# Kernel optimization log

Measured on AMD Instinct MI355X. Metric: run time of the kernel, lower is better.

## Reference

```python
import jax, jax.numpy as jnp
import numpy as np

N_NODES = 100000
N_EDGES = 640000
WIDTH = 128
LAYERS = 3
N_GRAPHS = 64


def setup_inputs() -> dict:
    key = jax.random.key(0)
    ks = jax.random.split(key, 6)
    x = jax.random.normal(ks[0], (N_NODES, WIDTH), dtype=jnp.float32)
    edge_index = jax.random.randint(ks[1], (2, N_EDGES), 0, N_NODES, dtype=jnp.int64)
    edge_attr = jax.random.uniform(ks[2], (N_EDGES, 1), dtype=jnp.float32)
    batch = jnp.sort(jax.random.randint(ks[3], (N_NODES,), 0, N_GRAPHS, dtype=jnp.int64))
    Ws = jax.random.normal(ks[4], (LAYERS, WIDTH, WIDTH), dtype=jnp.float32) / np.sqrt(WIDTH)
    bs = jnp.zeros((LAYERS, WIDTH), dtype=jnp.float32)
    return {"x": x, "edge_index": edge_index, "edge_attr": edge_attr,
            "batch": batch, "Ws": Ws, "bs": bs}


def reference(x, edge_index, edge_attr, batch, Ws, bs):
    N = x.shape[0]
    ew = edge_attr.squeeze()  # [E]
    loop = jnp.arange(N)
    # add self-loops with fill_value=2.0 (improved=True)
    row = jnp.concatenate([edge_index[0], loop])
    col = jnp.concatenate([edge_index[1], loop])
    w = jnp.concatenate([ew, jnp.full((N,), 2.0, dtype=ew.dtype)])
    # symmetric gcn normalization: deg computed at target (col)
    deg = jax.ops.segment_sum(w, col, num_segments=N)
    dinv = jnp.where(deg > 0, jax.lax.rsqrt(deg), 0.0)
    norm = dinv[row] * w * dinv[col]  # [E+N]

    for l in range(LAYERS):
        h = x @ Ws[l]  # [N, WIDTH]
        msg = norm[:, None] * h[row]  # gather + scale
        x = jax.ops.segment_sum(msg, col, num_segments=N) + bs[l]

    # global mean pool over graphs
    sums = jax.ops.segment_sum(x, batch, num_segments=N_GRAPHS)
    counts = jax.ops.segment_sum(jnp.ones((N,), dtype=x.dtype), batch, num_segments=N_GRAPHS)
    return sums / jnp.maximum(counts, 1.0)[:, None]
```

## Files before the change

kernel.cpp:

```cpp
#include <hip/hip_runtime.h>
#include <hip/hip_fp16.h>
#include <cstddef>

#define N_NODES  100000
#define N_EDGES  640000
#define WIDTH    128
#define LAYERS   3
#define N_GRAPHS 64
#define ELL_K    40

#define GLOAD_LDS16(gsrc, ldst) \
  __builtin_amdgcn_global_load_lds( \
      (const __attribute__((address_space(1))) unsigned*)(gsrc), \
      (__attribute__((address_space(3))) unsigned*)(ldst), 16, 0, 0)

__device__ __forceinline__ float h2f(unsigned short h) {
  __half x; *reinterpret_cast<unsigned short*>(&x) = h;
  return __half2float(x);
}
__device__ __forceinline__ unsigned short f2h(float f) {
  __half h = __float2half_rn(f);
  return *reinterpret_cast<unsigned short*>(&h);
}


__global__ void k_init(int* __restrict__ cursor, float* __restrict__ deg) {
  int i = blockIdx.x * blockDim.x + threadIdx.x;
  if (i < N_NODES) { cursor[i] = 0; deg[i] = 0.f; }
}

__global__ void k_cd(const int* __restrict__ col, const float* __restrict__ ew,
                     float* __restrict__ deg) {
  int e = blockIdx.x * blockDim.x + threadIdx.x;
  if (e < N_EDGES) atomicAdd(&deg[col[e]], ew[e]);
}

__global__ void k_dinv_e(const float* __restrict__ deg, float* __restrict__ dinv) {
  int v = blockIdx.x * blockDim.x + threadIdx.x;
  if (v < N_NODES) {
    float d = 2.0f + deg[v];
    dinv[v] = (d > 0.0f) ? 1.0f / sqrtf(d) : 0.0f;
  }
}

__global__ void k_fill_ell(const int* __restrict__ row, const int* __restrict__ col,
                           const float* __restrict__ ew, const float* __restrict__ dinv,
                           int* __restrict__ cursor, int2* __restrict__ ell) {
  int e = blockIdx.x * blockDim.x + threadIdx.x;
  if (e < N_EDGES) {
    int r = row[e], c = col[e];
    float nrm = dinv[r] * ew[e] * dinv[c];
    int slot = atomicAdd(&cursor[r], 1);
    if (slot < ELL_K) {
      int2 pk; pk.x = c; pk.y = __float_as_int(nrm);
      ell[(size_t)r * ELL_K + slot] = pk;
    }
  }
}

__device__ __forceinline__ int lbound(const int* __restrict__ batch, int key) {
  int lo = 0, hi = N_NODES;
  while (lo < hi) { int m = (lo + hi) >> 1; if (batch[m] < key) lo = m + 1; else hi = m; }
  return lo;
}

__global__ void k_cntg(const int* __restrict__ batch, int* __restrict__ cntg,
                       float* __restrict__ invc) {
  int g = threadIdx.x;
  if (g < N_GRAPHS) {
    int lb = lbound(batch, g), ub = lbound(batch, g + 1);
    int c = ub - lb;
    cntg[g] = c;
    invc[g] = 1.0f / (float)max(c, 1);
  }
}

__global__ void k_pinit(const int* __restrict__ batch, const float* __restrict__ invc,
                        unsigned short* __restrict__ p) {
  const int total = N_NODES * 16;
  for (int i = blockIdx.x * blockDim.x + threadIdx.x; i < total;
       i += gridDim.x * blockDim.x) {
    int v = i >> 4, q = i & 15;
    int b = batch[v];
    ushort4 u;
    ((unsigned short*)&u)[0] = (q * 4 + 0 == b) ? f2h(invc[b]) : (unsigned short)0;
    ((unsigned short*)&u)[1] = (q * 4 + 1 == b) ? f2h(invc[b]) : (unsigned short)0;
    ((unsigned short*)&u)[2] = (q * 4 + 2 == b) ? f2h(invc[b]) : (unsigned short)0;
    ((unsigned short*)&u)[3] = (q * 4 + 3 == b) ? f2h(invc[b]) : (unsigned short)0;
    ((ushort4*)p)[i] = u;
  }
}

#define CS_BLOCKS 512
__global__ __launch_bounds__(256) void k_colsum(
    const unsigned short* __restrict__ y, float* __restrict__ partc) {
  __shared__ float4 sd[256];
  int t = threadIdx.x;
  int slot = t & 15;
  int vrow = t >> 4;
  const int chunk = (N_NODES + CS_BLOCKS - 1) / CS_BLOCKS;
  int start = blockIdx.x * chunk;
  int end = min(start + chunk, N_NODES);
  float4 acc = {0.f, 0.f, 0.f, 0.f};
  for (int v = start + vrow; v < end; v += 16) {
    ushort4 u = ((const ushort4*)(y + (size_t)v * 64))[slot];
    acc.x += h2f(u.x); acc.y += h2f(u.y);
    acc.z += h2f(u.z); acc.w += h2f(u.w);
  }
  sd[t] = acc;
  __syncthreads();
  for (int off = 8; off > 0; off >>= 1) {
    if (vrow < off) {
      float4 o = sd[(vrow + off) * 16 + slot];
      acc.x += o.x; acc.y += o.y; acc.z += o.z; acc.w += o.w;
      sd[t] = acc;
    }
    __syncthreads();
  }
  if (vrow == 0)
    ((float4*)(partc + (size_t)blockIdx.x * 64))[slot] = acc;
}

__global__ __launch_bounds__(256) void k_cs2(
    const float* __restrict__ csA, const float* __restrict__ csB,
    float* __restrict__ ps, float* __restrict__ pas) {
  __shared__ float sd[256];
  const float* src = (blockIdx.x == 0) ? csA : csB;
  float* dst = (blockIdx.x == 0) ? ps : pas;
  int t = threadIdx.x;
  int g = t & 63, c = t >> 6;
  float a = 0.f;
  for (int r = c * 128; r < (c + 1) * 128; r++) a += src[r * 64 + g];
  sd[t] = a;
  __syncthreads();
  if (t < 128) sd[t] += sd[t + 128];
  __syncthreads();
  if (t < 64) dst[t] = sd[t] + sd[t + 64];
}

#define AGG_NPB 4
__global__ __launch_bounds__(256) void k_yagg(
    const unsigned short* __restrict__ yin, const int* __restrict__ cnt_a,
    const int2* __restrict__ ell, const float* __restrict__ dinv,
    unsigned short* __restrict__ yout) {
  int wave = threadIdx.x >> 6;
  int lane = threadIdx.x & 63;
  int v = blockIdx.x * AGG_NPB + wave;
  if (v >= N_NODES) return;
  int vv = __builtin_amdgcn_readfirstlane(v);
  int grp = lane >> 4;
  int q = lane & 15;

  ushort4 hvu = ((const ushort4*)(yin + (size_t)vv * 64))[q];
  int cnt = cnt_a[vv];

  float4 a0 = {0,0,0,0}, a1 = {0,0,0,0}, a2 = {0,0,0,0}, a3 = {0,0,0,0};
  int2 pk = (lane < cnt) ? ell[(size_t)vv * ELL_K + lane] : make_int2(0, 0);
  int   si = pk.x;
  float swv = __int_as_float(pk.y);

  for (int base = 0; base < cnt; base += 16) {
    int e0 = base + grp;
    float w0 = __shfl(swv, e0); int i0 = __shfl(si, e0);
    ushort4 u0 = ((const ushort4*)(yin + (size_t)i0 * 64))[q];
    a0.x += w0 * h2f(u0.x); a0.y += w0 * h2f(u0.y);
    a0.z += w0 * h2f(u0.z); a0.w += w0 * h2f(u0.w);
    if (base + 4 < cnt) {
      int e1 = base + 4 + grp;
      float w1 = __shfl(swv, e1); int i1 = __shfl(si, e1);
      ushort4 u1 = ((const ushort4*)(yin + (size_t)i1 * 64))[q];
      a1.x += w1 * h2f(u1.x); a1.y += w1 * h2f(u1.y);
      a1.z += w1 * h2f(u1.z); a1.w += w1 * h2f(u1.w);
    }
    if (base + 8 < cnt) {
      int e2 = base + 8 + grp;
      int e3 = base + 12 + grp;
      float w2 = __shfl(swv, e2); int i2 = __shfl(si, e2);
      float w3 = __shfl(swv, e3); int i3 = __shfl(si, e3);
      ushort4 u2 = ((const ushort4*)(yin + (size_t)i2 * 64))[q];
      ushort4 u3 = ((const ushort4*)(yin + (size_t)i3 * 64))[q];
      a2.x += w2 * h2f(u2.x); a2.y += w2 * h2f(u2.y);
      a2.z += w2 * h2f(u2.z); a2.w += w2 * h2f(u2.w);
      a3.x += w3 * h2f(u3.x); a3.y += w3 * h2f(u3.y);
      a3.z += w3 * h2f(u3.z); a3.w += w3 * h2f(u3.w);
    }
  }

  a0.x += a1.x + a2.x + a3.x;
  a0.y += a1.y + a2.y + a3.y;
  a0.z += a1.z + a2.z + a3.z;
  a0.w += a1.w + a2.w + a3.w;
#pragma unroll
  for (int d = 16; d <= 32; d <<= 1) {
    a0.x += __shfl_xor(a0.x, d);
    a0.y += __shfl_xor(a0.y, d);
    a0.z += __shfl_xor(a0.z, d);
    a0.w += __shfl_xor(a0.w, d);
  }

  if (grp == 0) {
    float dv = dinv[vv];
    float sc = 2.0f * dv * dv;
    ushort4 r;
    r.x = f2h(a0.x + sc * h2f(hvu.x));
    r.y = f2h(a0.y + sc * h2f(hvu.y));
    r.z = f2h(a0.z + sc * h2f(hvu.z));
    r.w = f2h(a0.w + sc * h2f(hvu.w));
    ((ushort4*)(yout + (size_t)vv * 64))[q] = r;
  }
}

#define CT_BLOCKS 768
#define CT_NCHUNK ((N_NODES + 63) / 64)

__global__ __launch_bounds__(256) void k_contract(
    const float* __restrict__ x0, const unsigned short* __restrict__ y3,
    float* __restrict__ part) {
  __shared__ __align__(16) float xs[64 * 128];
  __shared__ __align__(16) unsigned short ysh[64 * 64];
  int t = threadIdx.x;
  int w = t >> 6;
  int lane = t & 63;
  int j = lane * 2;

  float2 acc[16];
#pragma unroll
  for (int i = 0; i < 16; i++) acc[i] = make_float2(0.f, 0.f);

  for (int c = blockIdx.x; c < CT_NCHUNK; c += gridDim.x) {
    int cc = min(64, N_NODES - c * 64);
    int bx = cc * 512;
    int by = cc * 128;
    const char* gx = (const char*)(x0 + (size_t)c * 64 * 128);
    const char* gy = (const char*)(y3 + (size_t)c * 64 * 64);
    __syncthreads();
#pragma unroll
    for (int i = 0; i < 8; i++) {
      int off = i * 4096 + t * 16;
      if (off < bx) GLOAD_LDS16(gx + off, (char*)xs + off);
    }
#pragma unroll
    for (int i = 0; i < 2; i++) {
      int off = i * 4096 + t * 16;
      if (off < by) GLOAD_LDS16(gy + off, (char*)ysh + off);
    }
    asm volatile("s_waitcnt vmcnt(0)" ::: "memory");
    __syncthreads();

    for (int v = 0; v < cc; v++) {
      const ushort4* yr = (const ushort4*)(ysh + v * 64 + w * 16);
      ushort4 u0 = yr[0], u1 = yr[1], u2 = yr[2], u3 = yr[3];
      float2 xa = *(const float2*)(xs + v * 128 + j);
      float ys[16] = {h2f(u0.x), h2f(u0.y), h2f(u0.z), h2f(u0.w),
                      h2f(u1.x), h2f(u1.y), h2f(u1.z), h2f(u1.w),
                      h2f(u2.x), h2f(u2.y), h2f(u2.z), h2f(u2.w),
                      h2f(u3.x), h2f(u3.y), h2f(u3.z), h2f(u3.w)};
#pragma unroll
      for (int i = 0; i < 16; i++) {
        acc[i].x += ys[i] * xa.x;
        acc[i].y += ys[i] * xa.y;
      }
    }
  }

  float* dst = part + (size_t)blockIdx.x * (N_GRAPHS * WIDTH);
#pragma unroll
  for (int i = 0; i < 16; i++)
    *(float2*)(dst + (w * 16 + i) * WIDTH + j) = acc[i];
}

#define RC_ROWS 64
#define RC_RG (CT_BLOCKS / RC_ROWS)

__global__ __launch_bounds__(256) void k_reduce1(
    const float* __restrict__ part, float* __restrict__ part2) {
  int bid = blockIdx.x, t = threadIdx.x;
  int rg = bid >> 5, colc = bid & 31;
  int idx = colc * 256 + t;
  const float* src = part + (size_t)rg * RC_ROWS * (N_GRAPHS * WIDTH) + idx;
  float a0 = 0.f, a1 = 0.f, a2 = 0.f, a3 = 0.f;
  for (int r = 0; r < RC_ROWS; r += 4) {
    a0 += src[(size_t)(r + 0) * (N_GRAPHS * WIDTH)];
    a1 += src[(size_t)(r + 1) * (N_GRAPHS * WIDTH)];
    a2 += src[(size_t)(r + 2) * (N_GRAPHS * WIDTH)];
    a3 += src[(size_t)(r + 3) * (N_GRAPHS * WIDTH)];
  }
  part2[rg * (N_GRAPHS * WIDTH) + idx] = (a0 + a1) + (a2 + a3);
}

__global__ __launch_bounds__(WIDTH) void k_mm128(
    const float* __restrict__ A, const float* __restrict__ B, float* __restrict__ O) {
  __shared__ float Ar[WIDTH];
  int r = blockIdx.x, j = threadIdx.x;
  Ar[j] = A[r * WIDTH + j];
  __syncthreads();
  float a = 0.f;
#pragma unroll 8
  for (int k = 0; k < WIDTH; k++) a += Ar[k] * B[k * WIDTH + j];
  O[r * WIDTH + j] = a;
}

__global__ __launch_bounds__(WIDTH) void k_c01(
    const float* __restrict__ b0, const float* __restrict__ T1,
    const float* __restrict__ b1, const float* __restrict__ W2,
    float* __restrict__ c0, float* __restrict__ c1) {
  __shared__ float s0[WIDTH], s1v[WIDTH];
  int j = threadIdx.x;
  s0[j] = b0[j]; s1v[j] = b1[j];
  __syncthreads();
  float a0 = 0.f, a1 = 0.f;
#pragma unroll 8
  for (int k = 0; k < WIDTH; k++) {
    a0 += s0[k] * T1[k * WIDTH + j];
    a1 += s1v[k] * W2[k * WIDTH + j];
  }
  c0[j] = a0; c1[j] = a1;
}

__global__ __launch_bounds__(WIDTH) void k_out(
    const float* __restrict__ part2, const float* __restrict__ Wp,
    const float* __restrict__ c0, const float* __restrict__ c1,
    const float* __restrict__ ps, const float* __restrict__ pas,
    const int* __restrict__ cntg, const float* __restrict__ b2,
    float* __restrict__ out) {
  __shared__ float Cr[WIDTH];
  int g = blockIdx.x, j = threadIdx.x;
  float cv = 0.f;
#pragma unroll
  for (int rg = 0; rg < RC_RG; rg++)
    cv += part2[rg * (N_GRAPHS * WIDTH) + g * WIDTH + j];
  Cr[j] = cv;
  __syncthreads();
  float a = pas[g] * c0[j] + ps[g] * c1[j] + ((cntg[g] > 0) ? b2[j] : 0.f);
#pragma unroll 8
  for (int k = 0; k < WIDTH; k++) a += Cr[k] * Wp[k * WIDTH + j];
  out[g * WIDTH + j] = a;
}


extern "C" void kernel_launch(void* const* d_in, const int* in_sizes, int n_in,
                              void* d_out, int out_size, void* d_ws, size_t ws_size,
                              hipStream_t stream) {
  const float* x   = (const float*)d_in[0];
  const int* row   = (const int*)d_in[1];
  const int* col   = row + N_EDGES;
  const float* ew  = (const float*)d_in[2];
  const int* batch = (const int*)d_in[3];
  const float* Ws  = (const float*)d_in[4];
  const float* bs  = (const float*)d_in[5];
  float* out = (float*)d_out;

  char* w = (char*)d_ws;
  float* dinv    = (float*)(w + 0);
  float* deg     = (float*)(w + 400128);
  int*   cursor  = (int*)(w + 800256);
  int*   cntg    = (int*)(w + 1200384);
  float* invc    = (float*)(w + 1200640);
  float* ps      = (float*)(w + 1200896);
  float* pas     = (float*)(w + 1201152);
  float* T1      = (float*)(w + 1201408);
  float* Wp      = (float*)(w + 1266944);
  float* c0      = (float*)(w + 1332480);
  float* c1      = (float*)(w + 1332992);
  int2*  ell     = (int2*)(w + 1333504);
  float* part    = (float*)(w + 33554432);
  float* part2   = (float*)(w + 58720256);
  unsigned short* yA = (unsigned short*)(w + 59113472);
  unsigned short* yB = (unsigned short*)(w + 71913472);
  float* csA     = (float*)(w + 84713472);
  float* csB     = (float*)(w + 84844544);

  int nb_n = (N_NODES + 255) / 256;
  int nb_e = (N_EDGES + 255) / 256;

  k_init  <<<nb_n, 256, 0, stream>>>(cursor, deg);
  k_cd    <<<nb_e, 256, 0, stream>>>(col, ew, deg);
  k_dinv_e<<<nb_n, 256, 0, stream>>>(deg, dinv);
  k_fill_ell<<<nb_e, 256, 0, stream>>>(row, col, ew, dinv, cursor, ell);

  k_cntg <<<1, 64, 0, stream>>>(batch, cntg, invc);
  k_pinit<<<2048, 256, 0, stream>>>(batch, invc, yA);

  int nb_y = (N_NODES + AGG_NPB - 1) / AGG_NPB;
  k_yagg  <<<nb_y, 256, 0, stream>>>(yA, cursor, ell, dinv, yB);
  k_colsum<<<CS_BLOCKS, 256, 0, stream>>>(yB, csA);
  k_yagg  <<<nb_y, 256, 0, stream>>>(yB, cursor, ell, dinv, yA);
  k_colsum<<<CS_BLOCKS, 256, 0, stream>>>(yA, csB);
  k_yagg  <<<nb_y, 256, 0, stream>>>(yA, cursor, ell, dinv, yB);

  k_cs2  <<<2, 256, 0, stream>>>(csA, csB, ps, pas);
  k_mm128<<<WIDTH, WIDTH, 0, stream>>>(Ws + 1 * WIDTH * WIDTH, Ws + 2 * WIDTH * WIDTH, T1);
  k_mm128<<<WIDTH, WIDTH, 0, stream>>>(Ws + 0 * WIDTH * WIDTH, T1, Wp);
  k_c01  <<<1, WIDTH, 0, stream>>>(bs, T1, bs + WIDTH, Ws + 2 * WIDTH * WIDTH, c0, c1);

  k_contract<<<CT_BLOCKS, 256, 0, stream>>>(x, yB, part);
  k_reduce1 <<<RC_RG * 32, 256, 0, stream>>>(part, part2);
  k_out     <<<N_GRAPHS, WIDTH, 0, stream>>>(part2, Wp, c0, c1, ps, pas, cntg,
                                             bs + 2 * WIDTH, out);
}
```

Measured before the change: 288.0 us.

## Factor degree normalization out of edges, fuse ELL build, simplify contraction

Stores raw edge weights in the ELL table and rescales the pooling vectors by dinv so each aggregation applies a single per-node scale (d2 or dinv) instead of per-edge norms. This lets the degree accumulation and the ELL fill share one edge pass, which removes a separate kernel. Column sums are corrected with sqrt(deg). The contraction kernel drops its LDS staging and reads x and y directly per node, two nodes per iteration, with more blocks. The risk is extra fp16 rounding from the changed scaling, plus a larger partial buffer to reduce.

Result: faster. 278.8 us (-3.2%).

```diff
diff --git a/kernel.cpp b/kernel.cpp
--- a/kernel.cpp
+++ b/kernel.cpp
@@ -9,11 +9,6 @@
 #define N_GRAPHS 64
 #define ELL_K    40
 
-#define GLOAD_LDS16(gsrc, ldst) \
-  __builtin_amdgcn_global_load_lds( \
-      (const __attribute__((address_space(1))) unsigned*)(gsrc), \
-      (__attribute__((address_space(3))) unsigned*)(ldst), 16, 0, 0)
-
 __device__ __forceinline__ float h2f(unsigned short h) {
   __half x; *reinterpret_cast<unsigned short*>(&x) = h;
   return __half2float(x);
@@ -29,32 +24,32 @@
   if (i < N_NODES) { cursor[i] = 0; deg[i] = 0.f; }
 }
 
-__global__ void k_cd(const int* __restrict__ col, const float* __restrict__ ew,
-                     float* __restrict__ deg) {
+__global__ void k_fill_cd(const int* __restrict__ row, const int* __restrict__ col,
+                          const float* __restrict__ ew,
+                          int* __restrict__ cursor, float* __restrict__ deg,
+                          int2* __restrict__ ell) {
   int e = blockIdx.x * blockDim.x + threadIdx.x;
-  if (e < N_EDGES) atomicAdd(&deg[col[e]], ew[e]);
-}
-
-__global__ void k_dinv_e(const float* __restrict__ deg, float* __restrict__ dinv) {
+  if (e < N_EDGES) {
+    int r = row[e], c = col[e];
+    float w = ew[e];
+    atomicAdd(&deg[c], w);
+    int slot = atomicAdd(&cursor[r], 1);
+    if (slot < ELL_K) {
+      int2 pk; pk.x = c; pk.y = __float_as_int(w);
+      ell[(size_t)r * ELL_K + slot] = pk;
+    }
+  }
+}
+
+__global__ void k_dinv_e(const float* __restrict__ deg, float* __restrict__ dinv,
+                         float* __restrict__ d2, float* __restrict__ sq) {
   int v = blockIdx.x * blockDim.x + threadIdx.x;
   if (v < N_NODES) {
     float d = 2.0f + deg[v];
-    dinv[v] = (d > 0.0f) ? 1.0f / sqrtf(d) : 0.0f;
-  }
-}
-
-__global__ void k_fill_ell(const int* __restrict__ row, const int* __restrict__ col,
-                           const float* __restrict__ ew, const float* __restrict__ dinv,
-                           int* __restrict__ cursor, int2* __restrict__ ell) {
-  int e = blockIdx.x * blockDim.x + threadIdx.x;
-  if (e < N_EDGES) {
-    int r = row[e], c = col[e];
-    float nrm = dinv[r] * ew[e] * dinv[c];
-    int slot = atomicAdd(&cursor[r], 1);
-    if (slot < ELL_K) {
-      int2 pk; pk.x = c; pk.y = __float_as_int(nrm);
-      ell[(size_t)r * ELL_K + slot] = pk;
-    }
+    float di = (d > 0.0f) ? 1.0f / sqrtf(d) : 0.0f;
+    dinv[v] = di;
+    d2[v] = di * di;
+    sq[v] = sqrtf(d);
   }
 }
 
@@ -76,24 +71,26 @@
 }
 
 __global__ void k_pinit(const int* __restrict__ batch, const float* __restrict__ invc,
-                        unsigned short* __restrict__ p) {
+                        const float* __restrict__ dinv, unsigned short* __restrict__ p) {
   const int total = N_NODES * 16;
   for (int i = blockIdx.x * blockDim.x + threadIdx.x; i < total;
        i += gridDim.x * blockDim.x) {
     int v = i >> 4, q = i & 15;
     int b = batch[v];
+    unsigned short val = f2h(invc[b] * dinv[v]);
     ushort4 u;
-    ((unsigned short*)&u)[0] = (q * 4 + 0 == b) ? f2h(invc[b]) : (unsigned short)0;
-    ((unsigned short*)&u)[1] = (q * 4 + 1 == b) ? f2h(invc[b]) : (unsigned short)0;
-    ((unsigned short*)&u)[2] = (q * 4 + 2 == b) ? f2h(invc[b]) : (unsigned short)0;
-    ((unsigned short*)&u)[3] = (q * 4 + 3 == b) ? f2h(invc[b]) : (unsigned short)0;
+    ((unsigned short*)&u)[0] = (q * 4 + 0 == b) ? val : (unsigned short)0;
+    ((unsigned short*)&u)[1] = (q * 4 + 1 == b) ? val : (unsigned short)0;
+    ((unsigned short*)&u)[2] = (q * 4 + 2 == b) ? val : (unsigned short)0;
+    ((unsigned short*)&u)[3] = (q * 4 + 3 == b) ? val : (unsigned short)0;
     ((ushort4*)p)[i] = u;
   }
 }
 
 #define CS_BLOCKS 512
 __global__ __launch_bounds__(256) void k_colsum(
-    const unsigned short* __restrict__ y, float* __restrict__ partc) {
+    const unsigned short* __restrict__ y, const float* __restrict__ sq,
+    float* __restrict__ partc) {
   __shared__ float4 sd[256];
   int t = threadIdx.x;
   int slot = t & 15;
@@ -104,8 +101,9 @@
   float4 acc = {0.f, 0.f, 0.f, 0.f};
   for (int v = start + vrow; v < end; v += 16) {
     ushort4 u = ((const ushort4*)(y + (size_t)v * 64))[slot];
-    acc.x += h2f(u.x); acc.y += h2f(u.y);
-    acc.z += h2f(u.z); acc.w += h2f(u.w);
+    float rd = sq[v];
+    acc.x += h2f(u.x) * rd; acc.y += h2f(u.y) * rd;
+    acc.z += h2f(u.z) * rd; acc.w += h2f(u.w) * rd;
   }
   sd[t] = acc;
   __syncthreads();
@@ -141,7 +139,7 @@
 #define AGG_NPB 4
 __global__ __launch_bounds__(256) void k_yagg(
     const unsigned short* __restrict__ yin, const int* __restrict__ cnt_a,
-    const int2* __restrict__ ell, const float* __restrict__ dinv,
+    const int2* __restrict__ ell, const float* __restrict__ scale,
     unsigned short* __restrict__ yout) {
   int wave = threadIdx.x >> 6;
   int lane = threadIdx.x & 63;
@@ -199,74 +197,70 @@
   }
 
   if (grp == 0) {
-    float dv = dinv[vv];
-    float sc = 2.0f * dv * dv;
+    float sc = scale[vv];
     ushort4 r;
-    r.x = f2h(a0.x + sc * h2f(hvu.x));
-    r.y = f2h(a0.y + sc * h2f(hvu.y));
-    r.z = f2h(a0.z + sc * h2f(hvu.z));
-    r.w = f2h(a0.w + sc * h2f(hvu.w));
+    r.x = f2h(sc * (a0.x + 2.0f * h2f(hvu.x)));
+    r.y = f2h(sc * (a0.y + 2.0f * h2f(hvu.y)));
+    r.z = f2h(sc * (a0.z + 2.0f * h2f(hvu.z)));
+    r.w = f2h(sc * (a0.w + 2.0f * h2f(hvu.w)));
     ((ushort4*)(yout + (size_t)vv * 64))[q] = r;
   }
 }
 
-#define CT_BLOCKS 768
-#define CT_NCHUNK ((N_NODES + 63) / 64)
+#define CT_BLOCKS 1024
 
 __global__ __launch_bounds__(256) void k_contract(
     const float* __restrict__ x0, const unsigned short* __restrict__ y3,
     float* __restrict__ part) {
-  __shared__ __align__(16) float xs[64 * 128];
-  __shared__ __align__(16) unsigned short ysh[64 * 64];
   int t = threadIdx.x;
-  int w = t >> 6;
-  int lane = t & 63;
-  int j = lane * 2;
-
-  float2 acc[16];
-#pragma unroll
-  for (int i = 0; i < 16; i++) acc[i] = make_float2(0.f, 0.f);
-
-  for (int c = blockIdx.x; c < CT_NCHUNK; c += gridDim.x) {
-    int cc = min(64, N_NODES - c * 64);
-    int bx = cc * 512;
-    int by = cc * 128;
-    const char* gx = (const char*)(x0 + (size_t)c * 64 * 128);
-    const char* gy = (const char*)(y3 + (size_t)c * 64 * 64);
-    __syncthreads();
+  int jq = t & 31;
+  int gg = t >> 5;
+
+  float4 acc[8];
+#pragma unroll
+  for (int i = 0; i < 8; i++) acc[i] = make_float4(0.f, 0.f, 0.f, 0.f);
+
+  int v = blockIdx.x;
+  for (; v + CT_BLOCKS < N_NODES; v += 2 * CT_BLOCKS) {
+    int v2 = v + CT_BLOCKS;
+    float4 xa = ((const float4*)(x0 + (size_t)v * WIDTH))[jq];
+    float4 xb = ((const float4*)(x0 + (size_t)v2 * WIDTH))[jq];
+    const ushort4* ya = (const ushort4*)(y3 + (size_t)v * 64 + gg * 8);
+    const ushort4* yb = (const ushort4*)(y3 + (size_t)v2 * 64 + gg * 8);
+    ushort4 ua0 = ya[0], ua1 = ya[1];
+    ushort4 ub0 = yb[0], ub1 = yb[1];
+    float yas[8] = {h2f(ua0.x), h2f(ua0.y), h2f(ua0.z), h2f(ua0.w),
+                    h2f(ua1.x), h2f(ua1.y), h2f(ua1.z), h2f(ua1.w)};
+    float ybs[8] = {h2f(ub0.x), h2f(ub0.y), h2f(ub0.z), h2f(ub0.w),
+                    h2f(ub1.x), h2f(ub1.y), h2f(ub1.z), h2f(ub1.w)};
 #pragma unroll
     for (int i = 0; i < 8; i++) {
-      int off = i * 4096 + t * 16;
-      if (off < bx) GLOAD_LDS16(gx + off, (char*)xs + off);
-    }
-#pragma unroll
-    for (int i = 0; i < 2; i++) {
-      int off = i * 4096 + t * 16;
-      if (off < by) GLOAD_LDS16(gy + off, (char*)ysh + off);
-    }
-    asm volatile("s_waitcnt vmcnt(0)" ::: "memory");
-    __syncthreads();
-
-    for (int v = 0; v < cc; v++) {
-      const ushort4* yr = (const ushort4*)(ysh + v * 64 + w * 16);
-      ushort4 u0 = yr[0], u1 = yr[1], u2 = yr[2], u3 = yr[3];
-      float2 xa = *(const float2*)(xs + v * 128 + j);
-      float ys[16] = {h2f(u0.x), h2f(u0.y), h2f(u0.z), h2f(u0.w),
-                      h2f(u1.x), h2f(u1.y), h2f(u1.z), h2f(u1.w),
-                      h2f(u2.x), h2f(u2.y), h2f(u2.z), h2f(u2.w),
-                      h2f(u3.x), h2f(u3.y), h2f(u3.z), h2f(u3.w)};
-#pragma unroll
-      for (int i = 0; i < 16; i++) {
-        acc[i].x += ys[i] * xa.x;
-        acc[i].y += ys[i] * xa.y;
-      }
+      acc[i].x += yas[i] * xa.x; acc[i].y += yas[i] * xa.y;
+      acc[i].z += yas[i] * xa.z; acc[i].w += yas[i] * xa.w;
+    }
+#pragma unroll
+    for (int i = 0; i < 8; i++) {
+      acc[i].x += ybs[i] * xb.x; acc[i].y += ybs[i] * xb.y;
+      acc[i].z += ybs[i] * xb.z; acc[i].w += ybs[i] * xb.w;
+    }
+  }
+  if (v < N_NODES) {
+    float4 xa = ((const float4*)(x0 + (size_t)v * WIDTH))[jq];
+    const ushort4* ya = (const ushort4*)(y3 + (size_t)v * 64 + gg * 8);
+    ushort4 ua0 = ya[0], ua1 = ya[1];
+    float yas[8] = {h2f(ua0.x), h2f(ua0.y), h2f(ua0.z), h2f(ua0.w),
+                    h2f(ua1.x), h2f(ua1.y), h2f(ua1.z), h2f(ua1.w)};
+#pragma unroll
+    for (int i = 0; i < 8; i++) {
+      acc[i].x += yas[i] * xa.x; acc[i].y += yas[i] * xa.y;
+      acc[i].z += yas[i] * xa.z; acc[i].w += yas[i] * xa.w;
     }
   }
 
   float* dst = part + (size_t)blockIdx.x * (N_GRAPHS * WIDTH);
 #pragma unroll
-  for (int i = 0; i < 16; i++)
-    *(float2*)(dst + (w * 16 + i) * WIDTH + j) = acc[i];
+  for (int i = 0; i < 8; i++)
+    *(float4*)(dst + (gg * 8 + i) * WIDTH + jq * 4) = acc[i];
 }
 
 #define RC_ROWS 64
@@ -352,40 +346,41 @@
 
   char* w = (char*)d_ws;
   float* dinv    = (float*)(w + 0);
-  float* deg     = (float*)(w + 400128);
-  int*   cursor  = (int*)(w + 800256);
-  int*   cntg    = (int*)(w + 1200384);
-  float* invc    = (float*)(w + 1200640);
-  float* ps      = (float*)(w + 1200896);
-  float* pas     = (float*)(w + 1201152);
-  float* T1      = (float*)(w + 1201408);
-  float* Wp      = (float*)(w + 1266944);
-  float* c0      = (float*)(w + 1332480);
-  float* c1      = (float*)(w + 1332992);
-  int2*  ell     = (int2*)(w + 1333504);
-  float* part    = (float*)(w + 33554432);
-  float* part2   = (float*)(w + 58720256);
-  unsigned short* yA = (unsigned short*)(w + 59113472);
-  unsigned short* yB = (unsigned short*)(w + 71913472);
-  float* csA     = (float*)(w + 84713472);
-  float* csB     = (float*)(w + 84844544);
+  float* d2      = (float*)(w + 400128);
+  float* sq      = (float*)(w + 800256);
+  float* deg     = (float*)(w + 1200384);
+  int*   cursor  = (int*)(w + 1600512);
+  int*   cntg    = (int*)(w + 2000640);
+  float* invc    = (float*)(w + 2000896);
+  float* ps      = (float*)(w + 2001152);
+  float* pas     = (float*)(w + 2001408);
+  float* T1      = (float*)(w + 2001664);
+  float* Wp      = (float*)(w + 2067200);
+  float* c0      = (float*)(w + 2132736);
+  float* c1      = (float*)(w + 2133248);
+  int2*  ell     = (int2*)(w + 2133760);
+  float* part    = (float*)(w + 34133760);
+  float* part2   = (float*)(w + 67688192);
+  unsigned short* yA = (unsigned short*)(w + 68212480);
+  unsigned short* yB = (unsigned short*)(w + 81012480);
+  float* csA     = (float*)(w + 93812480);
+  float* csB     = (float*)(w + 93943552);
 
   int nb_n = (N_NODES + 255) / 256;
   int nb_e = (N_EDGES + 255) / 256;
 
-  k_init  <<<nb_n, 256, 0, stream>>>(cursor, deg);
-  k_cd    <<<nb_e, 256, 0, stream>>>(col, ew, deg);
-  k_dinv_e<<<nb_n, 256, 0, stream>>>(deg, dinv);
-  k_fill_ell<<<nb_e, 256, 0, stream>>>(row, col, ew, dinv, cursor, ell);
+  k_init   <<<nb_n, 256, 0, stream>>>(cursor, deg);
+  k_fill_cd<<<nb_e, 256, 0, stream>>>(row, col, ew, cursor, deg, ell);
+  k_dinv_e <<<nb_n, 256, 0, stream>>>(deg, dinv, d2, sq);
 
   k_cntg <<<1, 64, 0, stream>>>(batch, cntg, invc);
-  k_pinit<<<2048, 256, 0, stream>>>(batch, invc, yA);
+  k_pinit<<<2048, 256, 0, stream>>>(batch, invc, dinv, yA);
 
   int nb_y = (N_NODES + AGG_NPB - 1) / AGG_NPB;
-  k_yagg  <<<nb_y, 256, 0, stream>>>(yA, cursor, ell, dinv, yB);
-  k_colsum<<<CS_BLOCKS, 256, 0, stream>>>(yB, csA);
-  k_yagg  <<<nb_y, 256, 0, stream>>>(yB, cursor, ell, dinv, yA);
-  k_colsum<<<CS_BLOCKS, 256, 0, stream>>>(yA, csB);
+  k_yagg  <<<nb_y, 256, 0, stream>>>(yA, cursor, ell, d2, yB);
+  k_colsum<<<CS_BLOCKS, 256, 0, stream>>>(yB, sq, csA);
+  k_yagg  <<<nb_y, 256, 0, stream>>>(yB, cursor, ell, d2, yA);
+  k_colsum<<<CS_BLOCKS, 256, 0, stream>>>(yA, sq, csB);
   k_yagg  <<<nb_y, 256, 0, stream>>>(yA, cursor, ell, dinv, yB);
 
   k_cs2  <<<2, 256, 0, stream>>>(csA, csB, ps, pas);
```
